# Kernel optimization log

Hardware: AMD Instinct MI355X
Metric: run time of the kernel (lower is better)

The kernel has to match this reference:

```python
import jax, jax.numpy as jnp
import numpy as np

B, L = 4096, 200
G_DIM, L_DIM, A_DIM, H = 64, 64, 8, 32
MAX_ACTION = 1.0


def _init(k, shape, fan_in):
    bound = 1.0 / np.sqrt(fan_in)
    return jax.random.uniform(k, shape, jnp.float32, -bound, bound)


def setup_inputs() -> dict:
    key = jax.random.key(0)
    ks = jax.random.split(key, 16)
    return dict(
        global_states=jax.random.normal(ks[0], (B, G_DIM), jnp.float32),
        local_states=jax.random.normal(ks[1], (B, L, L_DIM), jnp.float32),
        W_w=_init(ks[2], (H, G_DIM), G_DIM), W_b=_init(ks[3], (H,), G_DIM),
        U_w=_init(ks[4], (H, L_DIM), L_DIM), U_b=_init(ks[5], (H,), L_DIM),
        att_w=_init(ks[6], (1, 2 * H), 2 * H), att_b=_init(ks[7], (1,), 2 * H),
        l1_w=_init(ks[8], (256, 2 * H), 2 * H), l1_b=_init(ks[9], (256,), 2 * H),
        l2_w=_init(ks[10], (256, 256), 256), l2_b=_init(ks[11], (256,), 256),
        l3_w=_init(ks[12], (A_DIM, 256), 256), l3_b=_init(ks[13], (A_DIM,), 256),
    )


def reference(global_states, local_states, W_w, W_b, U_w, U_b,
              att_w, att_b, l1_w, l1_b, l2_w, l2_b, l3_w, l3_b):
    h = W_w.shape[0]  # 32
    wg = global_states @ W_w.T + W_b                              # [B,H]
    ul = jnp.einsum('bld,hd->blh', local_states, U_w) + U_b       # [B,L,H]
    # att input row0 = cat(wg, wg); rows 1..L = cat(wg, ul)
    a_g, a_l = att_w[0, :h], att_w[0, h:]
    g_term = wg @ a_g                                             # [B]
    s0 = jax.nn.leaky_relu(g_term + wg @ a_l + att_b[0])          # [B]
    sl = jax.nn.leaky_relu(g_term[:, None] + ul @ a_l + att_b[0]) # [B,L]
    # normalize by sum (not softmax), matching torch.div(score, score.sum())
    total = s0 + sl.sum(axis=1)                                   # [B]
    n0 = s0 / total                                               # [B]
    nl = sl / total[:, None]                                      # [B,L]
    agg_local = jnp.einsum('bl,blh->bh', nl, ul)                  # [B,H]
    states = jax.nn.relu(jnp.concatenate([n0[:, None] * wg, agg_local], axis=1))  # [B,2H]
    a = jax.nn.relu(states @ l1_w.T + l1_b)
    a = jax.nn.relu(a @ l2_w.T + l2_b)
    a = jax.nn.sigmoid(a @ l3_w.T + l3_b)
    return MAX_ACTION * a
```

## Files before the change

### kernel.cpp

```cpp
#include <hip/hip_runtime.h>
#include <math.h>

#define BB 4096
#define LL 200
#define HH 32
#define PF 8


template<int CTRL>
__device__ __forceinline__ float dpp_ror_add(float x)
{
    int y = __builtin_amdgcn_update_dpp(0, __float_as_int(x),
                                        CTRL, 0xF, 0xF, true);
    return x + __int_as_float(y);
}

__global__ __launch_bounds__(256) void actor_fused_kernel(
    const float* __restrict__ gs,
    const float* __restrict__ ls,
    const float* __restrict__ W_w, const float* __restrict__ W_b,
    const float* __restrict__ U_w, const float* __restrict__ U_b,
    const float* __restrict__ att_w, const float* __restrict__ att_b,
    const float* __restrict__ l1_w, const float* __restrict__ l1_b,
    const float* __restrict__ l2_w, const float* __restrict__ l2_b,
    const float* __restrict__ l3_w, const float* __restrict__ l3_b,
    float* __restrict__ out)
{
    __shared__ float c_lds[4 * 64];
    __shared__ float y_lds[4 * 64];
    __shared__ __align__(16) float s_x [4 * 64];
    __shared__ __align__(16) float s_a1[4 * 260];
    __shared__ __align__(16) float s_a2[4 * 260];

    const int tid  = threadIdx.x;
    const int lane = tid & 63;
    const int wid  = tid >> 6;
    const int b    = blockIdx.x * 4 + wid;

    const int h    = lane & 31;
    const int half = lane >> 5;
    const int q    = lane & 15;
    const int lg   = lane >> 4;


    const float4* g4 = (const float4*)(gs + (size_t)b * 64);
    const float4* W4 = (const float4*)(W_w);
    float wg = (half == 0) ? W_b[h] : 0.f;
    #pragma unroll
    for (int dd = 0; dd < 8; ++dd) {
        float4 gv = g4[half * 8 + dd];
        float4 wv = W4[h * 16 + half * 8 + dd];
        wg += gv.x * wv.x + gv.y * wv.y + gv.z * wv.z + gv.w * wv.w;
    }
    wg += __shfl_xor(wg, 32);

    float gt = wg * att_w[h];
    float t2 = wg * att_w[HH + h];
    #pragma unroll
    for (int m = 1; m < 32; m <<= 1) {
        gt += __shfl_xor(gt, m);
        t2 += __shfl_xor(t2, m);
    }
    const float attb = att_b[0];
    const float lin0 = gt + t2 + attb;
    const float s0   = (lin0 > 0.f) ? lin0 : 0.01f * lin0;

    float c = 0.f;
    float ubal = 0.f;
    #pragma unroll
    for (int hh = 0; hh < HH; ++hh) {
        const float alh = att_w[HH + hh];
        c    += alh * U_w[hh * 64 + lane];
        ubal += alh * U_b[hh];
    }
    c_lds[wid * 64 + lane] = c;
    __syncthreads();
    const float4 cq = *(const float4*)&c_lds[wid * 64 + 4 * q];
    const float base = gt + ubal + attb;

    const float4* xs = (const float4*)(ls + (size_t)b * (LL * 64));
    const int idx0 = lg * 16 + q;
    float4 yx = make_float4(0.f, 0.f, 0.f, 0.f);
    float Sacc = 0.f;

    float4 Xbuf[PF];
    #pragma unroll
    for (int i = 0; i < PF; ++i)
        Xbuf[i] = xs[idx0 + i * 64];

    #pragma unroll
    for (int t = 0; t < 50; ++t) {
        float4 X = Xbuf[t & (PF - 1)];
        int tn = t + PF;
        if (tn > 49) tn = 49;
        Xbuf[t & (PF - 1)] = xs[idx0 + tn * 64];

        float p = X.x * cq.x + X.y * cq.y + X.z * cq.z + X.w * cq.w;
        p = dpp_ror_add<0x121>(p);
        p = dpp_ror_add<0x122>(p);
        p = dpp_ror_add<0x124>(p);
        p = dpp_ror_add<0x128>(p);
        const float linv = p + base;
        const float sl = (linv > 0.f) ? linv : 0.01f * linv;
        yx.x += sl * X.x;
        yx.y += sl * X.y;
        yx.z += sl * X.z;
        yx.w += sl * X.w;
        Sacc += sl;
    }

    #pragma unroll
    for (int m = 16; m < 64; m <<= 1) {
        yx.x += __shfl_xor(yx.x, m);
        yx.y += __shfl_xor(yx.y, m);
        yx.z += __shfl_xor(yx.z, m);
        yx.w += __shfl_xor(yx.w, m);
        Sacc += __shfl_xor(Sacc, m);
    }
    if (lane < 16) *(float4*)&y_lds[wid * 64 + 4 * q] = yx;
    __syncthreads();

    float V = (half == 0) ? (U_b[h] * Sacc) : 0.f;
    const float4* U4 = (const float4*)U_w;
    const float4* y4 = (const float4*)&y_lds[wid * 64];
    #pragma unroll
    for (int dd = 0; dd < 8; ++dd) {
        float4 uv = U4[h * 16 + half * 8 + dd];
        float4 yv = y4[half * 8 + dd];
        V += uv.x * yv.x + uv.y * yv.y + uv.z * yv.z + uv.w * yv.w;
    }
    V += __shfl_xor(V, 32);

    const float total = s0 + Sacc;
    const float n0    = s0 / total;
    const float outv  = (lane < 32) ? (n0 * wg) : (V / total);
    s_x[wid * 64 + lane] = fmaxf(outv, 0.f);
    __syncthreads();

    const int kl  = lane & 15;
    const int lgb = lane >> 4;

    {
        float4 xr[4];
        #pragma unroll
        for (int r = 0; r < 4; ++r)
            xr[r] = *(const float4*)&s_x[r * 64 + kl * 4];

        #pragma unroll
        for (int i = 0; i < 16; ++i) {
            const int u = (wid << 6) + (i << 2) + lgb;
            const float4 wv = *(const float4*)(l1_w + u * 64 + kl * 4);
            const float bias = l1_b[u];
            #pragma unroll
            for (int r = 0; r < 4; ++r) {
                float acc = wv.x * xr[r].x + wv.y * xr[r].y
                          + wv.z * xr[r].z + wv.w * xr[r].w;
                acc = dpp_ror_add<0x121>(acc);
                acc = dpp_ror_add<0x122>(acc);
                acc = dpp_ror_add<0x124>(acc);
                acc = dpp_ror_add<0x128>(acc);
                if (kl == 0)
                    s_a1[r * 260 + u] = fmaxf(acc + bias, 0.f);
            }
        }
    }
    __syncthreads();

    {
        float4 a1r[4][4];
        #pragma unroll
        for (int r = 0; r < 4; ++r)
            #pragma unroll
            for (int s = 0; s < 4; ++s)
                a1r[r][s] = *(const float4*)&s_a1[r * 260 + s * 64 + kl * 4];

        #pragma unroll
        for (int i = 0; i < 16; ++i) {
            const int u = (wid << 6) + (i << 2) + lgb;
            const float* wr = l2_w + (size_t)u * 256;
            const float4 wv0 = *(const float4*)(wr +   0 + kl * 4);
            const float4 wv1 = *(const float4*)(wr +  64 + kl * 4);
            const float4 wv2 = *(const float4*)(wr + 128 + kl * 4);
            const float4 wv3 = *(const float4*)(wr + 192 + kl * 4);
            const float bias = l2_b[u];
            #pragma unroll
            for (int r = 0; r < 4; ++r) {
                float acc = wv0.x * a1r[r][0].x + wv0.y * a1r[r][0].y
                          + wv0.z * a1r[r][0].z + wv0.w * a1r[r][0].w;
                acc      += wv1.x * a1r[r][1].x + wv1.y * a1r[r][1].y
                          + wv1.z * a1r[r][1].z + wv1.w * a1r[r][1].w;
                acc      += wv2.x * a1r[r][2].x + wv2.y * a1r[r][2].y
                          + wv2.z * a1r[r][2].z + wv2.w * a1r[r][2].w;
                acc      += wv3.x * a1r[r][3].x + wv3.y * a1r[r][3].y
                          + wv3.z * a1r[r][3].z + wv3.w * a1r[r][3].w;
                acc = dpp_ror_add<0x121>(acc);
                acc = dpp_ror_add<0x122>(acc);
                acc = dpp_ror_add<0x124>(acc);
                acc = dpp_ror_add<0x128>(acc);
                if (kl == 0)
                    s_a2[r * 260 + u] = fmaxf(acc + bias, 0.f);
            }
        }
    }
    __syncthreads();

    if (tid < 32) {
        int r = tid >> 3, o = tid & 7;
        float acc = l3_b[o];
        const float4* wr4 = (const float4*)(l3_w + o * 256);
        const float4* a4  = (const float4*)&s_a2[r * 260];
        #pragma unroll 8
        for (int k = 0; k < 64; ++k) {
            float4 av = a4[k];
            float4 wv = wr4[k];
            acc += av.x * wv.x + av.y * wv.y + av.z * wv.z + av.w * wv.w;
        }
        out[(size_t)(blockIdx.x * 4 + r) * 8 + o] =
            1.f / (1.f + __expf(-acc));
    }
}

extern "C" void kernel_launch(void* const* d_in, const int* in_sizes, int n_in,
                              void* d_out, int out_size, void* d_ws, size_t ws_size,
                              hipStream_t stream)
{
    const float* gs    = (const float*)d_in[0];
    const float* ls    = (const float*)d_in[1];
    const float* W_w   = (const float*)d_in[2];
    const float* W_b   = (const float*)d_in[3];
    const float* U_w   = (const float*)d_in[4];
    const float* U_b   = (const float*)d_in[5];
    const float* att_w = (const float*)d_in[6];
    const float* att_b = (const float*)d_in[7];
    const float* l1_w  = (const float*)d_in[8];
    const float* l1_b  = (const float*)d_in[9];
    const float* l2_w  = (const float*)d_in[10];
    const float* l2_b  = (const float*)d_in[11];
    const float* l3_w  = (const float*)d_in[12];
    const float* l3_b  = (const float*)d_in[13];

    actor_fused_kernel<<<BB / 4, 256, 0, stream>>>(
        gs, ls, W_w, W_b, U_w, U_b, att_w, att_b,
        l1_w, l1_b, l2_w, l2_b, l3_w, l3_b, (float*)d_out);
}
```

Baseline: 352.9 us.

## Split each row's local-state stream across two waves and double block size

Result: faster. 340.0 us (-3.6%).

```diff
diff --git a/kernel.cpp b/kernel.cpp
--- a/kernel.cpp
+++ b/kernel.cpp
@@ -4,7 +4,7 @@
 #define BB 4096
 #define LL 200
 #define HH 32
-#define PF 8
+#define PF 5
 
 
 template<int CTRL>
@@ -15,7 +15,7 @@
     return x + __int_as_float(y);
 }
 
-__global__ __launch_bounds__(256) void actor_fused_kernel(
+__global__ __launch_bounds__(512, 4) void actor_fused_kernel(
     const float* __restrict__ gs,
     const float* __restrict__ ls,
     const float* __restrict__ W_w, const float* __restrict__ W_b,
@@ -26,8 +26,9 @@
     const float* __restrict__ l3_w, const float* __restrict__ l3_b,
     float* __restrict__ out)
 {
-    __shared__ float c_lds[4 * 64];
-    __shared__ float y_lds[4 * 64];
+    __shared__ float c_lds[64];
+    __shared__ __align__(16) float y_part[8][64];
+    __shared__ float S_part[8];
     __shared__ __align__(16) float s_x [4 * 64];
     __shared__ __align__(16) float s_a1[4 * 260];
     __shared__ __align__(16) float s_a2[4 * 260];
@@ -35,12 +36,13 @@
     const int tid  = threadIdx.x;
     const int lane = tid & 63;
     const int wid  = tid >> 6;
-    const int b    = blockIdx.x * 4 + wid;
+    const int rblk = wid >> 1;
+    const int hpart= wid & 1;
+    const int b    = blockIdx.x * 4 + rblk;
 
     const int h    = lane & 31;
     const int half = lane >> 5;
     const int q    = lane & 15;
-    const int lg   = lane >> 4;
 
 
     const float4* g4 = (const float4*)(gs + (size_t)b * 64);
@@ -73,27 +75,26 @@
         c    += alh * U_w[hh * 64 + lane];
         ubal += alh * U_b[hh];
     }
-    c_lds[wid * 64 + lane] = c;
-    __syncthreads();
-    const float4 cq = *(const float4*)&c_lds[wid * 64 + 4 * q];
+    c_lds[lane] = c;
+    __syncthreads();
+    const float4 cq = *(const float4*)&c_lds[4 * q];
     const float base = gt + ubal + attb;
 
     const float4* xs = (const float4*)(ls + (size_t)b * (LL * 64));
-    const int idx0 = lg * 16 + q;
+    const int c0 = hpart * 25;
     float4 yx = make_float4(0.f, 0.f, 0.f, 0.f);
     float Sacc = 0.f;
 
     float4 Xbuf[PF];
     #pragma unroll
     for (int i = 0; i < PF; ++i)
-        Xbuf[i] = xs[idx0 + i * 64];
-
-    #pragma unroll
-    for (int t = 0; t < 50; ++t) {
-        float4 X = Xbuf[t & (PF - 1)];
-        int tn = t + PF;
-        if (tn > 49) tn = 49;
-        Xbuf[t & (PF - 1)] = xs[idx0 + tn * 64];
+        Xbuf[i] = xs[(c0 + i) * 64 + lane];
+
+    #pragma unroll
+    for (int t = 0; t < 25; ++t) {
+        float4 X = Xbuf[t % PF];
+        if (t < 25 - PF)
+            Xbuf[t % PF] = xs[(c0 + t + PF) * 64 + lane];
 
         float p = X.x * cq.x + X.y * cq.y + X.z * cq.z + X.w * cq.w;
         p = dpp_ror_add<0x121>(p);
@@ -117,24 +118,31 @@
         yx.w += __shfl_xor(yx.w, m);
         Sacc += __shfl_xor(Sacc, m);
     }
-    if (lane < 16) *(float4*)&y_lds[wid * 64 + 4 * q] = yx;
-    __syncthreads();
-
-    float V = (half == 0) ? (U_b[h] * Sacc) : 0.f;
-    const float4* U4 = (const float4*)U_w;
-    const float4* y4 = (const float4*)&y_lds[wid * 64];
-    #pragma unroll
-    for (int dd = 0; dd < 8; ++dd) {
-        float4 uv = U4[h * 16 + half * 8 + dd];
-        float4 yv = y4[half * 8 + dd];
-        V += uv.x * yv.x + uv.y * yv.y + uv.z * yv.z + uv.w * yv.w;
-    }
-    V += __shfl_xor(V, 32);
-
-    const float total = s0 + Sacc;
-    const float n0    = s0 / total;
-    const float outv  = (lane < 32) ? (n0 * wg) : (V / total);
-    s_x[wid * 64 + lane] = fmaxf(outv, 0.f);
+    if (lane < 16) *(float4*)&y_part[wid][4 * q] = yx;
+    if (lane == 0) S_part[wid] = Sacc;
+    __syncthreads();
+
+    if (!hpart) {
+        const float Stot = S_part[wid] + S_part[wid + 1];
+        float V = (half == 0) ? (U_b[h] * Stot) : 0.f;
+        const float4* U4  = (const float4*)U_w;
+        const float4* ya4 = (const float4*)&y_part[wid][0];
+        const float4* yb4 = (const float4*)&y_part[wid + 1][0];
+        #pragma unroll
+        for (int dd = 0; dd < 8; ++dd) {
+            float4 uv = U4[h * 16 + half * 8 + dd];
+            float4 va = ya4[half * 8 + dd];
+            float4 vb = yb4[half * 8 + dd];
+            V += uv.x * (va.x + vb.x) + uv.y * (va.y + vb.y)
+               + uv.z * (va.z + vb.z) + uv.w * (va.w + vb.w);
+        }
+        V += __shfl_xor(V, 32);
+
+        const float total = s0 + Stot;
+        const float n0    = s0 / total;
+        const float outv  = (lane < 32) ? (n0 * wg) : (V / total);
+        s_x[rblk * 64 + lane] = fmaxf(outv, 0.f);
+    }
     __syncthreads();
 
     const int kl  = lane & 15;
@@ -147,8 +155,8 @@
             xr[r] = *(const float4*)&s_x[r * 64 + kl * 4];
 
         #pragma unroll
-        for (int i = 0; i < 16; ++i) {
-            const int u = (wid << 6) + (i << 2) + lgb;
+        for (int i = 0; i < 8; ++i) {
+            const int u = (wid << 5) + (i << 2) + lgb;
             const float4 wv = *(const float4*)(l1_w + u * 64 + kl * 4);
             const float bias = l1_b[u];
             #pragma unroll
@@ -167,16 +175,9 @@
     __syncthreads();
 
     {
-        float4 a1r[4][4];
-        #pragma unroll
-        for (int r = 0; r < 4; ++r)
-            #pragma unroll
-            for (int s = 0; s < 4; ++s)
-                a1r[r][s] = *(const float4*)&s_a1[r * 260 + s * 64 + kl * 4];
-
-        #pragma unroll
-        for (int i = 0; i < 16; ++i) {
-            const int u = (wid << 6) + (i << 2) + lgb;
+        #pragma unroll
+        for (int i = 0; i < 8; ++i) {
+            const int u = (wid << 5) + (i << 2) + lgb;
             const float* wr = l2_w + (size_t)u * 256;
             const float4 wv0 = *(const float4*)(wr +   0 + kl * 4);
             const float4 wv1 = *(const float4*)(wr +  64 + kl * 4);
@@ -185,14 +186,14 @@
             const float bias = l2_b[u];
             #pragma unroll
             for (int r = 0; r < 4; ++r) {
-                float acc = wv0.x * a1r[r][0].x + wv0.y * a1r[r][0].y
-                          + wv0.z * a1r[r][0].z + wv0.w * a1r[r][0].w;
-                acc      += wv1.x * a1r[r][1].x + wv1.y * a1r[r][1].y
-                          + wv1.z * a1r[r][1].z + wv1.w * a1r[r][1].w;
-                acc      += wv2.x * a1r[r][2].x + wv2.y * a1r[r][2].y
-                          + wv2.z * a1r[r][2].z + wv2.w * a1r[r][2].w;
-                acc      += wv3.x * a1r[r][3].x + wv3.y * a1r[r][3].y
-                          + wv3.z * a1r[r][3].z + wv3.w * a1r[r][3].w;
+                const float4 a0 = *(const float4*)&s_a1[r * 260 +   0 + kl * 4];
+                const float4 a1 = *(const float4*)&s_a1[r * 260 +  64 + kl * 4];
+                const float4 a2 = *(const float4*)&s_a1[r * 260 + 128 + kl * 4];
+                const float4 a3 = *(const float4*)&s_a1[r * 260 + 192 + kl * 4];
+                float acc = wv0.x * a0.x + wv0.y * a0.y + wv0.z * a0.z + wv0.w * a0.w;
+                acc      += wv1.x * a1.x + wv1.y * a1.y + wv1.z * a1.z + wv1.w * a1.w;
+                acc      += wv2.x * a2.x + wv2.y * a2.y + wv2.z * a2.z + wv2.w * a2.w;
+                acc      += wv3.x * a3.x + wv3.y * a3.y + wv3.z * a3.z + wv3.w * a3.w;
                 acc = dpp_ror_add<0x121>(acc);
                 acc = dpp_ror_add<0x122>(acc);
                 acc = dpp_ror_add<0x124>(acc);
@@ -239,7 +240,7 @@
     const float* l3_w  = (const float*)d_in[12];
     const float* l3_b  = (const float*)d_in[13];
 
-    actor_fused_kernel<<<BB / 4, 256, 0, stream>>>(
+    actor_fused_kernel<<<BB / 4, 512, 0, stream>>>(
         gs, ls, W_w, W_b, U_w, U_b, att_w, att_b,
         l1_w, l1_b, l2_w, l2_b, l3_w, l3_b, (float*)d_out);
 }
```
